# Kernel tuning notes

Measured on AMD Instinct MI355X. Metric: run time of the kernel, lower is better.

## Reference

```python
import jax, jax.numpy as jnp
import numpy as np
import math

NUM_HEADS = 16
NUM_KV_HEADS = 4
HEAD_DIM = 128


def rotate_half(x):
    x1, x2 = x[..., : x.shape[-1] // 2], x[..., x.shape[-1] // 2 :]
    return jnp.concatenate((-x2, x1), axis=-1)


def setup_inputs() -> dict:
    key = jax.random.key(0)
    ks = jax.random.split(key, 7)
    B, L, D = 2, 2048, 2048
    hidden_states = jax.random.normal(ks[0], (B, L, D), dtype=jnp.float32)
    # realistic RoPE tables
    inv_freq = 1.0 / (10000.0 ** (np.arange(0, HEAD_DIM, 2, dtype=np.float32) / HEAD_DIM))
    t = np.arange(L, dtype=np.float32)
    freqs = np.outer(t, inv_freq)
    emb = np.concatenate([freqs, freqs], axis=-1)
    cos = jnp.asarray(np.cos(emb), dtype=jnp.float32)
    sin = jnp.asarray(np.sin(emb), dtype=jnp.float32)
    s = 1.0 / math.sqrt(D)
    Wq = jax.random.normal(ks[1], (D, NUM_HEADS * HEAD_DIM), dtype=jnp.float32) * s
    Wk = jax.random.normal(ks[2], (D, NUM_KV_HEADS * HEAD_DIM), dtype=jnp.float32) * s
    Wv = jax.random.normal(ks[3], (D, NUM_KV_HEADS * HEAD_DIM), dtype=jnp.float32) * s
    Wo = jax.random.normal(ks[4], (NUM_HEADS * HEAD_DIM, D), dtype=jnp.float32) * s
    return {"hidden_states": hidden_states, "cos": cos, "sin": sin,
            "Wq": Wq, "Wk": Wk, "Wv": Wv, "Wo": Wo}


def reference(hidden_states, cos, sin, Wq, Wk, Wv, Wo):
    B, L, D = hidden_states.shape
    H, KVH, Dh = NUM_HEADS, NUM_KV_HEADS, HEAD_DIM
    q = (hidden_states @ Wq).reshape(B, L, H, Dh)
    k = (hidden_states @ Wk).reshape(B, L, KVH, Dh)
    v = (hidden_states @ Wv).reshape(B, L, KVH, Dh)
    # RoPE: cos/sin are [L, Dh] broadcast over batch and heads
    c = cos[None, :, None, :]
    s = sin[None, :, None, :]
    q = q * c + rotate_half(q) * s
    k = k * c + rotate_half(k) * s
    # GQA: repeat kv heads to match query heads
    rep = H // KVH
    k = jnp.repeat(k, rep, axis=2)
    v = jnp.repeat(v, rep, axis=2)
    scale = 1.0 / math.sqrt(Dh)
    # [B, H, L, L]
    attn = jnp.einsum('bqhd,bkhd->bhqk', q, k) * scale
    i = jnp.arange(L)[:, None]
    j = jnp.arange(L)[None, :]
    attn = jnp.where(i >= j, attn, -jnp.inf)
    attn = jax.nn.softmax(attn, axis=-1)
    out = jnp.einsum('bhqk,bkhd->bqhd', attn, v).reshape(B, L, H * Dh)
    return out @ Wo
```

## Files before the change

kernel.cpp:

```cpp
#include <hip/hip_runtime.h>
#include <hip/hip_bf16.h>

typedef __attribute__((ext_vector_type(8))) short bf16x8;
typedef __attribute__((ext_vector_type(4))) float f32x4;
typedef __attribute__((ext_vector_type(4))) short short4v;

__device__ __forceinline__ unsigned short f2bf(float f) {
  union { float f; unsigned u; } x; x.f = f;
  return (unsigned short)((x.u + 0x7FFFu + ((x.u >> 16) & 1u)) >> 16);
}

__device__ __forceinline__ short f2bf_hw(float f) {
  __hip_bfloat16 h = __float2bfloat16(f);
  return *(short*)&h;
}

__device__ __forceinline__ void lds_cp16(const void* g, void* l) {
  __builtin_amdgcn_global_load_lds(
      (const __attribute__((address_space(1))) void*)g,
      (__attribute__((address_space(3))) void*)l,
      16, 0, 0);
}

#define GBAR() do { __builtin_amdgcn_s_barrier(); __builtin_amdgcn_sched_barrier(0); } while (0)

__global__ __launch_bounds__(256) void cast_x(const float* __restrict__ in,
                                              short* __restrict__ out, int n4) {
  int i = blockIdx.x * 256 + threadIdx.x;
  if (i >= n4) return;
  float4 v = reinterpret_cast<const float4*>(in)[i];
  short4v o;
  o.x = (short)f2bf(v.x); o.y = (short)f2bf(v.y);
  o.z = (short)f2bf(v.z); o.w = (short)f2bf(v.w);
  reinterpret_cast<short4v*>(out)[i] = o;
}

__global__ __launch_bounds__(256) void transp_cast(const float* __restrict__ in,
                                                   short* __restrict__ out,
                                                   int K, int N) {
  __shared__ float t[32][33];
  int bn = blockIdx.x * 32, bk = blockIdx.y * 32;
  int tx = threadIdx.x, ty = threadIdx.y;
  for (int i = ty; i < 32; i += 8)
    t[i][tx] = in[(size_t)(bk + i) * N + bn + tx];
  __syncthreads();
  for (int i = ty; i < 32; i += 8)
    out[(size_t)(bn + i) * K + bk + tx] = (short)f2bf(t[tx][i]);
}

__global__ __launch_bounds__(256) void transp_v(const short* __restrict__ V,
                                                short* __restrict__ VTo) {
  __shared__ short t[32][34];
  const int hd = blockIdx.z;
  const int p0 = blockIdx.x * 32, d0 = blockIdx.y * 32;
  const short* src = V + (size_t)hd * 2048 * 128;
  short* dst = VTo + (size_t)hd * 2048 * 128;
  int tx = threadIdx.x, ty = threadIdx.y;
  for (int i = ty; i < 32; i += 8)
    t[i][tx] = src[(size_t)(p0 + i) * 128 + d0 + tx];
  __syncthreads();
  for (int i = ty; i < 32; i += 8)
    dst[(size_t)(d0 + i) * 2048 + p0 + tx] = t[tx][i];
}

template <int BM, int EPI>
__global__ __launch_bounds__(512, 2) void gemm8p(
    const short* __restrict__ A, const short* __restrict__ Bt,
    float* __restrict__ C,
    short* __restrict__ Qo, short* __restrict__ Ko, short* __restrict__ Vo,
    const float* __restrict__ cosT, const float* __restrict__ sinT,
    int N, int Kd, int nbm) {
  constexpr int NM = BM / 64;
  __shared__ __align__(16) short As[2][BM * 64];
  __shared__ __align__(16) short Bs[2][256 * 64];
  const int tid = threadIdx.x;
  const int l = tid & 63, l15 = l & 15, l4 = l >> 4;
  const int wid = tid >> 6, wr = wid >> 1, wc = wid & 1;
  const int cpx = gridDim.x >> 3;
  const int sid = (blockIdx.x & 7) * cpx + (blockIdx.x >> 3);
  const int bm = sid % nbm, bn = sid / nbm;

  const int srow = tid >> 3;
  const int sch = tid & 7;

  auto stA = [&](int dbuf, int k0, int i) {
    const int rl = srow + i * 64;
    const int c = sch ^ (rl & 7);
    lds_cp16(A + (size_t)(bm * BM + rl) * Kd + k0 + c * 8,
             (char*)As[dbuf] + tid * 16 + i * 8192);
  };
  auto stB = [&](int dbuf, int k0, int j) {
    const int rl = srow + j * 64;
    const int c = sch ^ (rl & 7);
    lds_cp16(Bt + (size_t)(bn * 256 + rl) * Kd + k0 + c * 8,
             (char*)Bs[dbuf] + tid * 16 + j * 8192);
  };
  auto rdA = [&](int dbuf, int m, int kb) {
    const int row = wr * (BM / 4) + m * 16 + l15;
    return *(const bf16x8*)((const char*)As[dbuf] + (row << 7) +
                            ((kb * 64 + l4 * 16) ^ ((row & 7) << 4)));
  };
  auto rdB = [&](int dbuf, int nh, int f, int kb) {
    const int row = wc * 128 + nh * 64 + f * 16 + l15;
    return *(const bf16x8*)((const char*)Bs[dbuf] + (row << 7) +
                            ((kb * 64 + l4 * 16) ^ ((row & 7) << 4)));
  };

  f32x4 acc[NM][8];
#pragma unroll
  for (int m = 0; m < NM; m++)
#pragma unroll
    for (int n = 0; n < 8; n++) acc[m][n] = (f32x4){0.f, 0.f, 0.f, 0.f};

  const int NT = Kd >> 6;

#pragma unroll
  for (int i = 0; i < NM; i++) stA(0, 0, i);
#pragma unroll
  for (int j = 0; j < 4; j++) stB(0, 0, j);
  asm volatile("s_waitcnt vmcnt(0)" ::: "memory");
  GBAR();

  for (int kt = 0; kt < NT; kt++) {
    const int buf = kt & 1, nbf = buf ^ 1;
    const bool stg = (kt + 1 < NT);
    const int k1 = (kt + 1) << 6;
    bf16x8 a[NM], b[4];

#pragma unroll
    for (int m = 0; m < NM; m++) a[m] = rdA(buf, m, 0);
#pragma unroll
    for (int f = 0; f < 4; f++) b[f] = rdB(buf, 0, f, 0);
    if (stg) { stA(nbf, k1, 0); stA(nbf, k1, 1); }
    if (stg) asm volatile("s_waitcnt vmcnt(2)" ::: "memory");
    else     asm volatile("s_waitcnt vmcnt(0)" ::: "memory");
    GBAR();
    asm volatile("s_waitcnt lgkmcnt(0)" ::: "memory");
    __builtin_amdgcn_sched_barrier(0);
    __builtin_amdgcn_s_setprio(1);
#pragma unroll
    for (int m = 0; m < NM; m++)
#pragma unroll
      for (int f = 0; f < 4; f++)
        acc[m][f] = __builtin_amdgcn_mfma_f32_16x16x32_bf16(a[m], b[f], acc[m][f], 0, 0, 0);
    __builtin_amdgcn_s_setprio(0);
    GBAR();

#pragma unroll
    for (int f = 0; f < 4; f++) b[f] = rdB(buf, 1, f, 0);
    if (stg) {
      if (BM == 256) { stA(nbf, k1, 2); stA(nbf, k1, 3); }
      else           { stB(nbf, k1, 0); stB(nbf, k1, 2); }
    }
    GBAR();
    asm volatile("s_waitcnt lgkmcnt(0)" ::: "memory");
    __builtin_amdgcn_sched_barrier(0);
    __builtin_amdgcn_s_setprio(1);
#pragma unroll
    for (int m = 0; m < NM; m++)
#pragma unroll
      for (int f = 0; f < 4; f++)
        acc[m][4 + f] = __builtin_amdgcn_mfma_f32_16x16x32_bf16(a[m], b[f], acc[m][4 + f], 0, 0, 0);
    __builtin_amdgcn_s_setprio(0);
    GBAR();

#pragma unroll
    for (int m = 0; m < NM; m++) a[m] = rdA(buf, m, 1);
#pragma unroll
    for (int f = 0; f < 4; f++) b[f] = rdB(buf, 0, f, 1);
    if (stg) {
      if (BM == 256) { stB(nbf, k1, 0); stB(nbf, k1, 2); }
      else           { stB(nbf, k1, 1); stB(nbf, k1, 3); }
    }
    GBAR();
    asm volatile("s_waitcnt lgkmcnt(0)" ::: "memory");
    __builtin_amdgcn_sched_barrier(0);
    __builtin_amdgcn_s_setprio(1);
#pragma unroll
    for (int m = 0; m < NM; m++)
#pragma unroll
      for (int f = 0; f < 4; f++)
        acc[m][f] = __builtin_amdgcn_mfma_f32_16x16x32_bf16(a[m], b[f], acc[m][f], 0, 0, 0);
    __builtin_amdgcn_s_setprio(0);
    GBAR();

#pragma unroll
    for (int f = 0; f < 4; f++) b[f] = rdB(buf, 1, f, 1);
    if (stg && BM == 256) { stB(nbf, k1, 1); stB(nbf, k1, 3); }
    if (stg) asm volatile("s_waitcnt vmcnt(2)" ::: "memory");
    GBAR();
    asm volatile("s_waitcnt lgkmcnt(0)" ::: "memory");
    __builtin_amdgcn_sched_barrier(0);
    __builtin_amdgcn_s_setprio(1);
#pragma unroll
    for (int m = 0; m < NM; m++)
#pragma unroll
      for (int f = 0; f < 4; f++)
        acc[m][4 + f] = __builtin_amdgcn_mfma_f32_16x16x32_bf16(a[m], b[f], acc[m][4 + f], 0, 0, 0);
    __builtin_amdgcn_s_setprio(0);
    GBAR();
  }

  if (EPI == 0) {
#pragma unroll
    for (int m = 0; m < NM; m++) {
      const int grow = bm * BM + wr * (BM / 4) + m * 16 + l4 * 4;
#pragma unroll
      for (int ni = 0; ni < 8; ni++) {
        const int col = bn * 256 + wc * 128 + (ni >> 2) * 64 + (ni & 3) * 16 + l15;
#pragma unroll
        for (int r = 0; r < 4; r++)
          C[(size_t)(grow + r) * N + col] = acc[m][ni][r];
      }
    }
  } else {
    const int head = bn * 2 + wc;
#pragma unroll
    for (int m = 0; m < NM; m++) {
#pragma unroll
      for (int r = 0; r < 4; r++) {
        const int grow = bm * BM + wr * (BM / 4) + m * 16 + l4 * 4 + r;
        const int bb = grow >> 11, pos = grow & 2047;
        if (head < 20) {
          float c4[4], s4[4];
#pragma unroll
          for (int ni = 0; ni < 4; ni++) {
            const int dh = ni * 16 + l15;
            c4[ni] = cosT[pos * 128 + dh];
            s4[ni] = sinT[pos * 128 + dh];
          }
          short* dst;
          if (head < 16) dst = Qo + ((size_t)(bb * 16 + head) * 2048 + pos) * 128;
          else           dst = Ko + ((size_t)(bb * 4 + (head - 16)) * 2048 + pos) * 128;
#pragma unroll
          for (int ni = 0; ni < 4; ni++) {
            const int dh = ni * 16 + l15;
            float xlo = acc[m][ni][r], xhi = acc[m][ni + 4][r];
            dst[dh]      = (short)f2bf(xlo * c4[ni] - xhi * s4[ni]);
            dst[dh + 64] = (short)f2bf(xhi * c4[ni] + xlo * s4[ni]);
          }
        } else {
          short* dst = Vo + ((size_t)(bb * 4 + (head - 20)) * 2048 + pos) * 128;
#pragma unroll
          for (int ni = 0; ni < 8; ni++)
            dst[(ni >> 2) * 64 + (ni & 3) * 16 + l15] = (short)f2bf(acc[m][ni][r]);
        }
      }
    }
  }
}

__global__ __launch_bounds__(256) void attn_fwd(
    const short* __restrict__ Q, const short* __restrict__ K,
    const short* __restrict__ VT, short* __restrict__ AO) {
  __shared__ __align__(16) short Ks[2][32 * 128];
  __shared__ __align__(16) short VTs[2][128 * 32];
  __shared__ __align__(16) short Pl[4][16 * 32];
  const int tid = threadIdx.x;
  const int w = tid >> 6, l = tid & 63;
  const int l15 = l & 15, l4 = l >> 4;
  const int bh = blockIdx.x;
  const int qt = 31 - blockIdx.y;
  const int b = bh >> 4, h = bh & 15, kv = h >> 2;
  const short* Qbase = Q + (size_t)(b * 16 + h) * 2048 * 128;
  const short* Kbase = K + (size_t)(b * 4 + kv) * 2048 * 128;
  const short* VTb   = VT + (size_t)(b * 4 + kv) * 2048 * 128;

  const int rkA = tid >> 4,          ckA = (tid & 15) ^ (rkA & 7);
  const int rkB = (tid + 256) >> 4,  ckB = (tid & 15) ^ (rkB & 7);
  const int rpA = tid >> 2,         rvA = rpA ^ ((rpA >> 3) & 1), cvA = (tid & 3) ^ ((rvA >> 1) & 3);
  const int rpB = (tid + 256) >> 2, rvB = rpB ^ ((rpB >> 3) & 1), cvB = (tid & 3) ^ ((rvB >> 1) & 3);

  const float SCL = 0.08838834764831845f * 1.4426950408889634f;

  bf16x8 ones;
#pragma unroll
  for (int j = 0; j < 8; j++) ones[j] = (short)0x3F80;

  const int q0w = qt * 64 + w * 16;

  bf16x8 qf[4];
#pragma unroll
  for (int kb = 0; kb < 4; kb++)
    qf[kb] = *(const bf16x8*)(Qbase + (size_t)(q0w + l15) * 128 + kb * 32 + l4 * 8);

  f32x4 oacc[8];
#pragma unroll
  for (int i = 0; i < 8; i++) oacc[i] = (f32x4){0.f, 0.f, 0.f, 0.f};
  f32x4 lacc = (f32x4){0.f, 0.f, 0.f, 0.f};

  const int ntiles = 2 * qt + 2;

  {
    lds_cp16(Kbase + (size_t)rkA * 128 + ckA * 8, (char*)Ks[0] + w * 1024);
    lds_cp16(Kbase + (size_t)rkB * 128 + ckB * 8, (char*)Ks[0] + 4096 + w * 1024);
    lds_cp16(VTb + (size_t)rvA * 2048 + cvA * 8,  (char*)VTs[0] + w * 1024);
    lds_cp16(VTb + (size_t)rvB * 2048 + cvB * 8,  (char*)VTs[0] + 4096 + w * 1024);
  }

  for (int nt = 0; nt < ntiles; nt++) {
    const int k0 = nt * 32, buf = nt & 1;
    __syncthreads();
    if (nt + 1 < ntiles) {
      const int kn = k0 + 32, bnx = buf ^ 1;
      lds_cp16(Kbase + (size_t)(kn + rkA) * 128 + ckA * 8, (char*)Ks[bnx] + w * 1024);
      lds_cp16(Kbase + (size_t)(kn + rkB) * 128 + ckB * 8, (char*)Ks[bnx] + 4096 + w * 1024);
      lds_cp16(VTb + (size_t)rvA * 2048 + kn + cvA * 8,    (char*)VTs[bnx] + w * 1024);
      lds_cp16(VTb + (size_t)rvB * 2048 + kn + cvB * 8,    (char*)VTs[bnx] + 4096 + w * 1024);
    }

    if (k0 <= q0w + 15) {
      f32x4 sa[2];
      sa[0] = (f32x4){0.f, 0.f, 0.f, 0.f};
      sa[1] = (f32x4){0.f, 0.f, 0.f, 0.f};
      __builtin_amdgcn_s_setprio(1);
#pragma unroll
      for (int kg = 0; kg < 2; kg++) {
        const int row = kg * 16 + l15;
        const int swz = (row & 7) << 4;
#pragma unroll
        for (int kb = 0; kb < 4; kb++) {
          const char* kp = (const char*)Ks[buf] + ((row * 256 + kb * 64 + l4 * 16) ^ swz);
          sa[kg] = __builtin_amdgcn_mfma_f32_16x16x32_bf16(qf[kb], *(const bf16x8*)kp, sa[kg], 0, 0, 0);
        }
      }
      __builtin_amdgcn_s_setprio(0);

      float p[2][4];
      const bool domask = (k0 + 31 > q0w);
#pragma unroll
      for (int kg = 0; kg < 2; kg++)
#pragma unroll
        for (int r = 0; r < 4; r++) {
          float pv = exp2f(sa[kg][r] * SCL);
          if (domask) {
            int qrow = q0w + l4 * 4 + r;
            if (k0 + kg * 16 + l15 > qrow) pv = 0.f;
          }
          p[kg][r] = pv;
        }

#pragma unroll
      for (int r = 0; r < 4; r++) {
        const int rw = l4 * 4 + r;
        const int swz = ((rw >> 1) & 7) << 4;
        *(short*)((char*)Pl[w] + ((rw * 64 + l15 * 2) ^ swz))      = f2bf_hw(p[0][r]);
        *(short*)((char*)Pl[w] + ((rw * 64 + 32 + l15 * 2) ^ swz)) = f2bf_hw(p[1][r]);
      }
      asm volatile("s_waitcnt lgkmcnt(0)" ::: "memory");
      bf16x8 pf = *(const bf16x8*)((const char*)Pl[w] + ((l15 * 64 + l4 * 16) ^ (((l15 >> 1) & 7) << 4)));

      __builtin_amdgcn_s_setprio(1);
#pragma unroll
      for (int nb = 0; nb < 8; nb++) {
        const int row = nb * 16 + l15;
        const char* vp = (const char*)VTs[buf] + ((row * 64 + l4 * 16) ^ (((row >> 1) & 7) << 4));
        oacc[nb] = __builtin_amdgcn_mfma_f32_16x16x32_bf16(pf, *(const bf16x8*)vp, oacc[nb], 0, 0, 0);
      }
      lacc = __builtin_amdgcn_mfma_f32_16x16x32_bf16(pf, ones, lacc, 0, 0, 0);
      __builtin_amdgcn_s_setprio(0);
    }
  }

#pragma unroll
  for (int r = 0; r < 4; r++) {
    float inv = 1.0f / lacc[r];
    size_t rowb = ((size_t)b * 2048 + q0w + l4 * 4 + r) * 2048 + h * 128;
#pragma unroll
    for (int nb = 0; nb < 8; nb++)
      AO[rowb + nb * 16 + l15] = f2bf_hw(oacc[nb][r] * inv);
  }
}

extern "C" void kernel_launch(void* const* d_in, const int* in_sizes, int n_in,
                              void* d_out, int out_size, void* d_ws, size_t ws_size,
                              hipStream_t stream) {
  const float* hs   = (const float*)d_in[0];
  const float* cosT = (const float*)d_in[1];
  const float* sinT = (const float*)d_in[2];
  const float* Wq   = (const float*)d_in[3];
  const float* Wk   = (const float*)d_in[4];
  const float* Wv   = (const float*)d_in[5];
  const float* Wo   = (const float*)d_in[6];
  float* out = (float*)d_out;

  char* p = (char*)d_ws;
  short* Xb   = (short*)p; p += (size_t)4096 * 2048 * 2;
  short* Wqkv = (short*)p; p += (size_t)3072 * 2048 * 2;
  short* Wot  = (short*)p; p += (size_t)2048 * 2048 * 2;
  short* Qb   = (short*)p; p += (size_t)2 * 16 * 2048 * 128 * 2;
  short* Kb   = (short*)p; p += (size_t)2 * 4 * 2048 * 128 * 2;
  short* Vb   = (short*)p; p += (size_t)2 * 4 * 2048 * 128 * 2;
  short* VTb  = (short*)p; p += (size_t)2 * 4 * 2048 * 128 * 2;
  short* AO   = Xb;

  cast_x<<<8192, 256, 0, stream>>>(hs, Xb, 2097152);
  transp_cast<<<dim3(64, 64), dim3(32, 8), 0, stream>>>(Wq, Wqkv, 2048, 2048);
  transp_cast<<<dim3(16, 64), dim3(32, 8), 0, stream>>>(Wk, Wqkv + (size_t)2048 * 2048, 2048, 512);
  transp_cast<<<dim3(16, 64), dim3(32, 8), 0, stream>>>(Wv, Wqkv + (size_t)2560 * 2048, 2048, 512);
  transp_cast<<<dim3(64, 64), dim3(32, 8), 0, stream>>>(Wo, Wot, 2048, 2048);

  gemm8p<256, 1><<<192, 512, 0, stream>>>(Xb, Wqkv, nullptr, Qb, Kb, Vb,
                                          cosT, sinT, 3072, 2048, 16);
  transp_v<<<dim3(64, 4, 8), dim3(32, 8), 0, stream>>>(Vb, VTb);
  attn_fwd<<<dim3(32, 32), 256, 0, stream>>>(Qb, Kb, VTb, AO);
  gemm8p<128, 0><<<256, 512, 0, stream>>>(AO, Wot, out, nullptr, nullptr, nullptr,
                                          nullptr, nullptr, 2048, 2048, 32);
}
```

Measured before the change: 240.3 us.

## Pair causal query tiles per block and widen attention KV tiles to 64

The attention kernel now launches 512 blocks, each handling two query tiles (pp and 31-pp) in turn, so every block does the same amount of causal work. KV tiles grow from 32 to 64 keys, with matching LDS buffers, swizzles and two P fragments per step, which halves barrier and loop overhead per key. A block-index remap groups blocks so that neighbours share K/V data in cache. In exchange, LDS use doubles, which may lower occupancy, and the diagonal tile wastes more masked work per wave.

```diff
diff --git a/kernel.cpp b/kernel.cpp
--- a/kernel.cpp
+++ b/kernel.cpp
@@ -253,23 +253,27 @@
 __global__ __launch_bounds__(256) void attn_fwd(
     const short* __restrict__ Q, const short* __restrict__ K,
     const short* __restrict__ VT, short* __restrict__ AO) {
-  __shared__ __align__(16) short Ks[2][32 * 128];
-  __shared__ __align__(16) short VTs[2][128 * 32];
-  __shared__ __align__(16) short Pl[4][16 * 32];
+  __shared__ __align__(16) short Ks[2][64 * 128];
+  __shared__ __align__(16) short VTs[2][128 * 64];
+  __shared__ __align__(16) short Pl[4][16 * 64];
   const int tid = threadIdx.x;
   const int w = tid >> 6, l = tid & 63;
   const int l15 = l & 15, l4 = l >> 4;
-  const int bh = blockIdx.x;
-  const int qt = 31 - blockIdx.y;
+  const int bid = blockIdx.x;
+  const int lg = (bid & 7) * 64 + (bid >> 3);
+  const int bh = lg >> 4, pp = lg & 15;
   const int b = bh >> 4, h = bh & 15, kv = h >> 2;
   const short* Qbase = Q + (size_t)(b * 16 + h) * 2048 * 128;
   const short* Kbase = K + (size_t)(b * 4 + kv) * 2048 * 128;
   const short* VTb   = VT + (size_t)(b * 4 + kv) * 2048 * 128;
 
-  const int rkA = tid >> 4,          ckA = (tid & 15) ^ (rkA & 7);
-  const int rkB = (tid + 256) >> 4,  ckB = (tid & 15) ^ (rkB & 7);
-  const int rpA = tid >> 2,         rvA = rpA ^ ((rpA >> 3) & 1), cvA = (tid & 3) ^ ((rvA >> 1) & 3);
-  const int rpB = (tid + 256) >> 2, rvB = rpB ^ ((rpB >> 3) & 1), cvB = (tid & 3) ^ ((rvB >> 1) & 3);
+  int rk[4], ck[4], dv[4], kc[4];
+#pragma unroll
+  for (int i = 0; i < 4; i++) {
+    const int c = tid + i * 256;
+    rk[i] = c >> 4; ck[i] = (c & 15) ^ (rk[i] & 7);
+    dv[i] = c >> 3; kc[i] = (c & 7) ^ (dv[i] & 7);
+  }
 
   const float SCL = 0.08838834764831845f * 1.4426950408889634f;
 
@@ -277,59 +281,63 @@
 #pragma unroll
   for (int j = 0; j < 8; j++) ones[j] = (short)0x3F80;
 
-  const int q0w = qt * 64 + w * 16;
-
-  bf16x8 qf[4];
-#pragma unroll
-  for (int kb = 0; kb < 4; kb++)
-    qf[kb] = *(const bf16x8*)(Qbase + (size_t)(q0w + l15) * 128 + kb * 32 + l4 * 8);
-
-  f32x4 oacc[8];
-#pragma unroll
-  for (int i = 0; i < 8; i++) oacc[i] = (f32x4){0.f, 0.f, 0.f, 0.f};
-  f32x4 lacc = (f32x4){0.f, 0.f, 0.f, 0.f};
-
-  const int ntiles = 2 * qt + 2;
-
-  {
-    lds_cp16(Kbase + (size_t)rkA * 128 + ckA * 8, (char*)Ks[0] + w * 1024);
-    lds_cp16(Kbase + (size_t)rkB * 128 + ckB * 8, (char*)Ks[0] + 4096 + w * 1024);
-    lds_cp16(VTb + (size_t)rvA * 2048 + cvA * 8,  (char*)VTs[0] + w * 1024);
-    lds_cp16(VTb + (size_t)rvB * 2048 + cvB * 8,  (char*)VTs[0] + 4096 + w * 1024);
-  }
-
-  for (int nt = 0; nt < ntiles; nt++) {
-    const int k0 = nt * 32, buf = nt & 1;
+  for (int qq = 0; qq < 2; qq++) {
+    const int qt = qq ? (31 - pp) : pp;
+    const int q0w = qt * 64 + w * 16;
+
+    bf16x8 qf[4];
+#pragma unroll
+    for (int kb = 0; kb < 4; kb++)
+      qf[kb] = *(const bf16x8*)(Qbase + (size_t)(q0w + l15) * 128 + kb * 32 + l4 * 8);
+
+    f32x4 oacc[8];
+#pragma unroll
+    for (int i = 0; i < 8; i++) oacc[i] = (f32x4){0.f, 0.f, 0.f, 0.f};
+    f32x4 lacc = (f32x4){0.f, 0.f, 0.f, 0.f};
+
+    const int ntiles = qt + 1;
+
     __syncthreads();
-    if (nt + 1 < ntiles) {
-      const int kn = k0 + 32, bnx = buf ^ 1;
-      lds_cp16(Kbase + (size_t)(kn + rkA) * 128 + ckA * 8, (char*)Ks[bnx] + w * 1024);
-      lds_cp16(Kbase + (size_t)(kn + rkB) * 128 + ckB * 8, (char*)Ks[bnx] + 4096 + w * 1024);
-      lds_cp16(VTb + (size_t)rvA * 2048 + kn + cvA * 8,    (char*)VTs[bnx] + w * 1024);
-      lds_cp16(VTb + (size_t)rvB * 2048 + kn + cvB * 8,    (char*)VTs[bnx] + 4096 + w * 1024);
-    }
-
-    if (k0 <= q0w + 15) {
-      f32x4 sa[2];
-      sa[0] = (f32x4){0.f, 0.f, 0.f, 0.f};
-      sa[1] = (f32x4){0.f, 0.f, 0.f, 0.f};
+#pragma unroll
+    for (int i = 0; i < 4; i++) {
+      lds_cp16(Kbase + (size_t)rk[i] * 128 + ck[i] * 8, (char*)Ks[0] + i * 4096 + tid * 16);
+      lds_cp16(VTb + (size_t)dv[i] * 2048 + kc[i] * 8,  (char*)VTs[0] + i * 4096 + tid * 16);
+    }
+
+    for (int nt = 0; nt < ntiles; nt++) {
+      const int k0 = nt * 64, buf = nt & 1;
+      __syncthreads();
+      if (nt + 1 < ntiles) {
+        const int kn = k0 + 64, bnx = buf ^ 1;
+#pragma unroll
+        for (int i = 0; i < 4; i++) {
+          lds_cp16(Kbase + (size_t)(kn + rk[i]) * 128 + ck[i] * 8,
+                   (char*)Ks[bnx] + i * 4096 + tid * 16);
+          lds_cp16(VTb + (size_t)dv[i] * 2048 + kn + kc[i] * 8,
+                   (char*)VTs[bnx] + i * 4096 + tid * 16);
+        }
+      }
+
+      f32x4 sa[4];
+#pragma unroll
+      for (int kg = 0; kg < 4; kg++) sa[kg] = (f32x4){0.f, 0.f, 0.f, 0.f};
       __builtin_amdgcn_s_setprio(1);
 #pragma unroll
-      for (int kg = 0; kg < 2; kg++) {
+      for (int kg = 0; kg < 4; kg++) {
         const int row = kg * 16 + l15;
         const int swz = (row & 7) << 4;
 #pragma unroll
         for (int kb = 0; kb < 4; kb++) {
-          const char* kp = (const char*)Ks[buf] + ((row * 256 + kb * 64 + l4 * 16) ^ swz);
+          const char* kp = (const char*)Ks[buf] + row * 256 + ((kb * 64 + l4 * 16) ^ swz);
           sa[kg] = __builtin_amdgcn_mfma_f32_16x16x32_bf16(qf[kb], *(const bf16x8*)kp, sa[kg], 0, 0, 0);
         }
       }
       __builtin_amdgcn_s_setprio(0);
 
-      float p[2][4];
-      const bool domask = (k0 + 31 > q0w);
-#pragma unroll
-      for (int kg = 0; kg < 2; kg++)
+      float p[4][4];
+      const bool domask = (k0 + 63 > q0w);
+#pragma unroll
+      for (int kg = 0; kg < 4; kg++)
 #pragma unroll
         for (int r = 0; r < 4; r++) {
           float pv = exp2f(sa[kg][r] * SCL);
@@ -343,32 +351,43 @@
 #pragma unroll
       for (int r = 0; r < 4; r++) {
         const int rw = l4 * 4 + r;
-        const int swz = ((rw >> 1) & 7) << 4;
-        *(short*)((char*)Pl[w] + ((rw * 64 + l15 * 2) ^ swz))      = f2bf_hw(p[0][r]);
-        *(short*)((char*)Pl[w] + ((rw * 64 + 32 + l15 * 2) ^ swz)) = f2bf_hw(p[1][r]);
+        const int swz = (rw & 7) << 4;
+#pragma unroll
+        for (int kg = 0; kg < 4; kg++)
+          *(short*)((char*)Pl[w] + (rw * 128 + ((kg * 32 + l15 * 2) ^ swz))) =
+              f2bf_hw(p[kg][r]);
       }
       asm volatile("s_waitcnt lgkmcnt(0)" ::: "memory");
-      bf16x8 pf = *(const bf16x8*)((const char*)Pl[w] + ((l15 * 64 + l4 * 16) ^ (((l15 >> 1) & 7) << 4)));
+      bf16x8 pf[2];
+#pragma unroll
+      for (int ks = 0; ks < 2; ks++)
+        pf[ks] = *(const bf16x8*)((const char*)Pl[w] +
+                 (l15 * 128 + ((ks * 64 + l4 * 16) ^ ((l15 & 7) << 4))));
 
       __builtin_amdgcn_s_setprio(1);
 #pragma unroll
       for (int nb = 0; nb < 8; nb++) {
-        const int row = nb * 16 + l15;
-        const char* vp = (const char*)VTs[buf] + ((row * 64 + l4 * 16) ^ (((row >> 1) & 7) << 4));
-        oacc[nb] = __builtin_amdgcn_mfma_f32_16x16x32_bf16(pf, *(const bf16x8*)vp, oacc[nb], 0, 0, 0);
-      }
-      lacc = __builtin_amdgcn_mfma_f32_16x16x32_bf16(pf, ones, lacc, 0, 0, 0);
+        const int d = nb * 16 + l15;
+        const int dsw = (d & 7) << 4;
+#pragma unroll
+        for (int ks = 0; ks < 2; ks++) {
+          const char* vp = (const char*)VTs[buf] + d * 128 + ((ks * 64 + l4 * 16) ^ dsw);
+          oacc[nb] = __builtin_amdgcn_mfma_f32_16x16x32_bf16(pf[ks], *(const bf16x8*)vp, oacc[nb], 0, 0, 0);
+        }
+      }
+      lacc = __builtin_amdgcn_mfma_f32_16x16x32_bf16(pf[0], ones, lacc, 0, 0, 0);
+      lacc = __builtin_amdgcn_mfma_f32_16x16x32_bf16(pf[1], ones, lacc, 0, 0, 0);
       __builtin_amdgcn_s_setprio(0);
     }
-  }
-
-#pragma unroll
-  for (int r = 0; r < 4; r++) {
-    float inv = 1.0f / lacc[r];
-    size_t rowb = ((size_t)b * 2048 + q0w + l4 * 4 + r) * 2048 + h * 128;
-#pragma unroll
-    for (int nb = 0; nb < 8; nb++)
-      AO[rowb + nb * 16 + l15] = f2bf_hw(oacc[nb][r] * inv);
+
+#pragma unroll
+    for (int r = 0; r < 4; r++) {
+      float inv = 1.0f / lacc[r];
+      size_t rowb = ((size_t)b * 2048 + q0w + l4 * 4 + r) * 2048 + h * 128;
+#pragma unroll
+      for (int nb = 0; nb < 8; nb++)
+        AO[rowb + nb * 16 + l15] = f2bf_hw(oacc[nb][r] * inv);
+    }
   }
 }
 
@@ -403,7 +422,7 @@
   gemm8p<256, 1><<<192, 512, 0, stream>>>(Xb, Wqkv, nullptr, Qb, Kb, Vb,
                                           cosT, sinT, 3072, 2048, 16);
   transp_v<<<dim3(64, 4, 8), dim3(32, 8), 0, stream>>>(Vb, VTb);
-  attn_fwd<<<dim3(32, 32), 256, 0, stream>>>(Qb, Kb, VTb, AO);
+  attn_fwd<<<512, 256, 0, stream>>>(Qb, Kb, VTb, AO);
   gemm8p<128, 0><<<256, 512, 0, stream>>>(AO, Wot, out, nullptr, nullptr, nullptr,
                                           nullptr, nullptr, 2048, 2048, 32);
 }
```

Result: faster. 220.8 us (-8.1%).
